# Optimization experiments

Hardware: AMD Instinct MI355X
Metric: run time of the kernel (lower is better)

Reference implementation:

```python
import jax, jax.numpy as jnp
import numpy as np

B, I, H1, H2, E, T = 16384, 512, 256, 128, 8, 2


def setup_inputs() -> dict:
    key = jax.random.key(0)
    ks = jax.random.split(key, 4)
    # Xavier-ish scaling for stability
    x = jax.random.normal(ks[0], (B, I), dtype=jnp.float32)
    W1 = jax.random.normal(ks[1], (E, I, H1), dtype=jnp.float32) / np.sqrt(I)
    b1 = jnp.zeros((E, H1), dtype=jnp.float32)
    W2 = jax.random.normal(ks[2], (E, H1, H2), dtype=jnp.float32) / np.sqrt(H1)
    b2 = jnp.zeros((E, H2), dtype=jnp.float32)
    Wg = jax.random.normal(ks[3], (T, I, E), dtype=jnp.float32) / np.sqrt(I)
    bg = jnp.zeros((T, E), dtype=jnp.float32)
    return {"x": x, "W1": W1, "b1": b1, "W2": W2, "b2": b2, "Wg": Wg, "bg": bg}


def reference(x, W1, b1, W2, b2, Wg, bg):
    # All experts as one grouped GEMM: [E, B, H1]
    h = jax.nn.relu(jnp.einsum('bi,eih->ebh', x, W1) + b1[:, None, :])
    # Last expert layer (lastlayer_reg=True -> act applied): [E, B, H2]
    e_out = jax.nn.relu(jnp.einsum('ebh,eho->ebo', h, W2) + b2[:, None, :])
    # Per-task gates with softmax over experts: [T, B, E]
    gates = jax.nn.softmax(jnp.einsum('bi,tie->tbe', x, Wg) + bg[:, None, :], axis=-1)
    # Gate-weighted combine of expert outputs: [T, B, H2]
    towers = jnp.einsum('tbe,ebo->tbo', gates, e_out)
    return towers
```

## Files before the change

kernel.cpp:

```cpp
#include <hip/hip_runtime.h>
#include <hip/hip_bf16.h>

#define B_  16384
#define I_  512
#define H1_ 256
#define H2_ 128
#define E_  8
#define T_  2

typedef __attribute__((ext_vector_type(8))) short short8;
typedef __attribute__((ext_vector_type(4))) float float4_t;

__device__ inline unsigned short f2bf(float f) {
    union { float f; unsigned u; } v; v.f = f;
    unsigned r = v.u + 0x7FFFu + ((v.u >> 16) & 1u);
    return (unsigned short)(r >> 16);
}

__device__ inline void async_copy16(const unsigned short* g, unsigned short* l) {
    __builtin_amdgcn_global_load_lds(
        (const __attribute__((address_space(1))) void*)g,
        (__attribute__((address_space(3))) void*)l,
        16, 0, 0);
}

__global__ void prep_gates_kernel(const float* __restrict__ x,
                                  unsigned short* __restrict__ xb,
                                  const float* __restrict__ W1,
                                  unsigned short* __restrict__ w1t,
                                  const float* __restrict__ W2,
                                  unsigned short* __restrict__ w2t,
                                  const float* __restrict__ Wg,
                                  const float* __restrict__ bg,
                                  float* __restrict__ gates) {
    __shared__ __align__(16) char smem[16 * 520 * 2 + 4 * 16 * 16 * 4];
    int bid = blockIdx.x;
    int t = threadIdx.x;

    if (bid < 1024) {
        unsigned short* wgtL = (unsigned short*)smem;
        float (*red)[16][16] = (float (*)[16][16])(smem + 16 * 520 * 2);
#pragma unroll
        for (int j = 0; j < 32; ++j) {
            int idx = j * 256 + t;
            int e = idx & 7, i = (idx >> 3) & 511, task = idx >> 12;
            wgtL[(task * 8 + e) * 520 + i] = f2bf(Wg[idx]);
        }
        __syncthreads();

        int w = t >> 6, lane = t & 63;
        int col = lane & 15, quad = lane >> 4;
        int b0 = bid * 16;
        int k0 = w * 128;
        const float* xr = x + (size_t)(b0 + col) * I_ + k0 + quad * 8;
        unsigned short* xw = xb + (size_t)(b0 + col) * I_ + k0 + quad * 8;
        const unsigned short* bL = &wgtL[col * 520 + k0 + quad * 8];
        float4_t acc = {0.f, 0.f, 0.f, 0.f};
#pragma unroll
        for (int ks = 0; ks < 128; ks += 32) {
            float4_t xa = *(const float4_t*)(xr + ks);
            float4_t xc = *(const float4_t*)(xr + ks + 4);
            short8 a;
            a[0] = (short)f2bf(xa[0]); a[1] = (short)f2bf(xa[1]);
            a[2] = (short)f2bf(xa[2]); a[3] = (short)f2bf(xa[3]);
            a[4] = (short)f2bf(xc[0]); a[5] = (short)f2bf(xc[1]);
            a[6] = (short)f2bf(xc[2]); a[7] = (short)f2bf(xc[3]);
            *(short8*)(xw + ks) = a;
            short8 b = *(const short8*)(bL + ks);
            acc = __builtin_amdgcn_mfma_f32_16x16x32_bf16(a, b, acc, 0, 0, 0);
        }
#pragma unroll
        for (int p = 0; p < 4; ++p)
            red[w][quad * 4 + p][col] = acc[p];
        __syncthreads();
        int r = t >> 4, te = t & 15;
        float v = red[0][r][te] + red[1][r][te] + red[2][r][te] + red[3][r][te] + bg[te];
        float m = v;
        m = fmaxf(m, __shfl_xor(m, 1));
        m = fmaxf(m, __shfl_xor(m, 2));
        m = fmaxf(m, __shfl_xor(m, 4));
        float ev = __expf(v - m);
        float s = ev;
        s += __shfl_xor(s, 1);
        s += __shfl_xor(s, 2);
        s += __shfl_xor(s, 4);
        gates[(size_t)te * B_ + b0 + r] = ev / s;
    } else {
        float (*tile)[33] = (float (*)[33])smem;
        const float* in; unsigned short* outp; int R, C, e, r0, c0;
        if (bid < 2048) {
            int tl = bid - 1024;
            e = tl >> 7; int rem = tl & 127;
            R = I_; C = H1_;
            r0 = (rem >> 3) * 32; c0 = (rem & 7) * 32;
            in = W1; outp = w1t;
        } else {
            int tl = bid - 2048;
            e = tl >> 5; int rem = tl & 31;
            R = H1_; C = H2_;
            r0 = (rem >> 2) * 32; c0 = (rem & 3) * 32;
            in = W2; outp = w2t;
        }
        const float* inp = in + (size_t)e * R * C;
        unsigned short* op = outp + (size_t)e * R * C;
        int tx = t & 31, ty = t >> 5;
#pragma unroll
        for (int j = 0; j < 32; j += 8)
            tile[ty + j][tx] = inp[(size_t)(r0 + ty + j) * C + c0 + tx];
        __syncthreads();
#pragma unroll
        for (int j = 0; j < 32; j += 8)
            op[(size_t)(c0 + ty + j) * R + r0 + tx] = f2bf(tile[tx][ty + j]);
    }
}

__global__ __launch_bounds__(512, 2)
void l1_gemm_kernel(const unsigned short* __restrict__ xb,
                    const unsigned short* __restrict__ w1t,
                    const float* __restrict__ b1,
                    unsigned short* __restrict__ h) {
    __shared__ __align__(16) unsigned short smem[65536];

    int bid = blockIdx.x;
    int wg = (bid & 7) * 64 + (bid >> 3);
    int m0 = (wg >> 3) * 256;
    int e  = wg & 7;

    int t = threadIdx.x, w = t >> 6, lane = t & 63;
    int col = lane & 15, quad = lane >> 4;
    int wm = (w & 1) * 128;
    int wn = (w >> 1) * 64;

    int rowA = w * 8 + (lane >> 3);
    int csw  = ((lane & 7) ^ (rowA & 7)) * 8;
    const unsigned short* aG = xb  + (size_t)(m0 + rowA) * I_ + csw;
    const unsigned short* bG = w1t + ((size_t)e * H1_ + rowA) * I_ + csw;

    unsigned short* AsBase = smem;
    unsigned short* BsBase = smem + 32768;
    int ldsw = w * 512;

    float4_t acc[8][4];
#pragma unroll
    for (int mf = 0; mf < 8; ++mf)
#pragma unroll
        for (int nf = 0; nf < 4; ++nf)
            acc[mf][nf] = (float4_t){0.f, 0.f, 0.f, 0.f};

#pragma unroll
    for (int p = 0; p < 4; ++p) {
        async_copy16(aG + ((size_t)p * 64) * I_, AsBase + p * 4096 + ldsw);
        async_copy16(bG + ((size_t)p * 64) * I_, BsBase + p * 4096 + ldsw);
    }

    short8 bf[4][2];

#pragma unroll 1
    for (int kt = 0; kt < 8; ++kt) {
        const int cur = kt & 1, nb = cur ^ 1;
        unsigned short* Ac = AsBase + cur * 16384;
        unsigned short* Bc = BsBase + cur * 16384;
        unsigned short* An = AsBase + nb * 16384;
        unsigned short* Bn = BsBase + nb * 16384;
        const unsigned short* aN = aG + (size_t)(kt + 1) * 64;
        const unsigned short* bN = bG + (size_t)(kt + 1) * 64;

        if (kt < 7) {
            async_copy16(aN, An + ldsw);
            async_copy16(bN, Bn + ldsw);
            asm volatile("s_waitcnt vmcnt(2)" ::: "memory");
        } else {
            asm volatile("s_waitcnt vmcnt(0)" ::: "memory");
        }
        asm volatile("s_barrier" ::: "memory");

#pragma unroll
        for (int nf = 0; nf < 4; ++nf) {
            int n = wn + nf * 16 + col;
#pragma unroll
            for (int kq = 0; kq < 2; ++kq) {
                int q = kq * 4 + quad;
                bf[nf][kq] = *(const short8*)&Bc[n * 64 + ((q ^ (n & 7)) << 3)];
            }
        }

#pragma unroll
        for (int p = 0; p < 4; ++p) {
            if (p > 0 && kt < 7) {
                async_copy16(aN + ((size_t)p * 64) * I_, An + p * 4096 + ldsw);
                async_copy16(bN + ((size_t)p * 64) * I_, Bn + p * 4096 + ldsw);
            }
            short8 af[2][2];
#pragma unroll
            for (int s = 0; s < 2; ++s) {
                int r = wm + (p * 2 + s) * 16 + col;
#pragma unroll
                for (int kq = 0; kq < 2; ++kq) {
                    int q = kq * 4 + quad;
                    af[s][kq] = *(const short8*)&Ac[r * 64 + ((q ^ (r & 7)) << 3)];
                }
            }
            asm volatile("s_waitcnt lgkmcnt(0)" ::: "memory");
            __builtin_amdgcn_sched_barrier(0);
            __builtin_amdgcn_s_setprio(1);
#pragma unroll
            for (int s = 0; s < 2; ++s)
#pragma unroll
                for (int nf = 0; nf < 4; ++nf)
#pragma unroll
                    for (int kq = 0; kq < 2; ++kq)
                        acc[p * 2 + s][nf] = __builtin_amdgcn_mfma_f32_16x16x32_bf16(
                            af[s][kq], bf[nf][kq], acc[p * 2 + s][nf], 0, 0, 0);
            __builtin_amdgcn_s_setprio(0);
            asm volatile("s_barrier" ::: "memory");
        }
    }

    unsigned short* Ct = smem;
    const float* bE = b1 + e * H1_;
#pragma unroll
    for (int half = 0; half < 2; ++half) {
        if ((w & 1) == half) {
#pragma unroll
            for (int mf = 0; mf < 8; ++mf) {
#pragma unroll
                for (int nf = 0; nf < 4; ++nf) {
                    int n = wn + nf * 16 + col;
                    float bv = bE[n];
#pragma unroll
                    for (int p2 = 0; p2 < 4; ++p2) {
                        float v = acc[mf][nf][p2] + bv;
                        v = v > 0.f ? v : 0.f;
                        Ct[(mf * 16 + quad * 4 + p2) * 264 + n] = f2bf(v);
                    }
                }
            }
        }
        __syncthreads();
        unsigned short* hrow = h + ((size_t)e * B_ + m0 + half * 128) * H1_;
#pragma unroll
        for (int j = 0; j < 8; ++j) {
            int idx = j * 512 + t;
            int row = idx >> 5, cc = idx & 31;
            short8 vv = *(const short8*)&Ct[row * 264 + cc * 8];
            *(short8*)&hrow[(size_t)row * H1_ + cc * 8] = vv;
        }
        __syncthreads();
    }
}

__global__ __launch_bounds__(512, 2)
void fused_l2_combine_kernel(const unsigned short* __restrict__ h,
                             const unsigned short* __restrict__ w2t,
                             const float* __restrict__ b2,
                             const float* __restrict__ gates,
                             float* __restrict__ out) {
    __shared__ unsigned short As[64 * 256];
    __shared__ unsigned short Bs[128 * 256];
    __shared__ float gL[16][64];

    int b0 = blockIdx.x * 64;
    int t = threadIdx.x, w = t >> 6, lane = t & 63;
    int col = lane & 15, quad = lane >> 4;
    int wm = (w & 1) * 32, wn = (w >> 1) * 32;

    if (t < 256) {
        int te = t >> 4, r4 = (t & 15) * 4;
        *(float4_t*)&gL[te][r4] = *(const float4_t*)&gates[(size_t)te * B_ + b0 + r4];
    }

    float4_t tw0[2][2], tw1[2][2];
#pragma unroll
    for (int mi = 0; mi < 2; ++mi)
#pragma unroll
        for (int ni = 0; ni < 2; ++ni) {
            tw0[mi][ni] = (float4_t){0.f, 0.f, 0.f, 0.f};
            tw1[mi][ni] = (float4_t){0.f, 0.f, 0.f, 0.f};
        }

    int rL = w * 2 + (lane >> 5);
    int cL = lane & 31;

    for (int e = 0; e < E_; ++e) {
        const unsigned short* hE  = h   + ((size_t)e * B_ + b0) * H1_;
        const unsigned short* w2E = w2t + (size_t)e * H2_ * H1_;

#pragma unroll
        for (int j = 0; j < 4; ++j) {
            int r = j * 16 + rL;
            int cg = (cL & 24) | ((cL ^ r) & 7);
            async_copy16(hE + (size_t)r * H1_ + cg * 8, As + j * 4096 + w * 512);
        }
#pragma unroll
        for (int j = 0; j < 8; ++j) {
            int r = j * 16 + rL;
            int cg = (cL & 24) | ((cL ^ r) & 7);
            async_copy16(w2E + (size_t)r * H1_ + cg * 8, Bs + j * 4096 + w * 512);
        }
        __syncthreads();

        float4_t acc[2][2];
#pragma unroll
        for (int mi = 0; mi < 2; ++mi)
#pragma unroll
            for (int ni = 0; ni < 2; ++ni)
                acc[mi][ni] = (float4_t){0.f, 0.f, 0.f, 0.f};

#pragma unroll
        for (int kk = 0; kk < 8; ++kk) {
            int c = kk * 4 + quad;
            short8 af[2], bfv[2];
#pragma unroll
            for (int mi = 0; mi < 2; ++mi) {
                int r = wm + mi * 16 + col;
                int l = (c & 24) | ((c ^ r) & 7);
                af[mi] = *(const short8*)&As[r * 256 + l * 8];
            }
#pragma unroll
            for (int ni = 0; ni < 2; ++ni) {
                int n = wn + ni * 16 + col;
                int l = (c & 24) | ((c ^ n) & 7);
                bfv[ni] = *(const short8*)&Bs[n * 256 + l * 8];
            }
#pragma unroll
            for (int mi = 0; mi < 2; ++mi)
#pragma unroll
                for (int ni = 0; ni < 2; ++ni)
                    acc[mi][ni] = __builtin_amdgcn_mfma_f32_16x16x32_bf16(
                        af[mi], bfv[ni], acc[mi][ni], 0, 0, 0);
        }
        __syncthreads();

#pragma unroll
        for (int ni = 0; ni < 2; ++ni) {
            float bv = b2[e * H2_ + wn + ni * 16 + col];
#pragma unroll
            for (int mi = 0; mi < 2; ++mi) {
#pragma unroll
                for (int p = 0; p < 4; ++p) {
                    int rloc = wm + mi * 16 + quad * 4 + p;
                    float v = acc[mi][ni][p] + bv;
                    v = v > 0.f ? v : 0.f;
                    tw0[mi][ni][p] += gL[e][rloc] * v;
                    tw1[mi][ni][p] += gL[8 + e][rloc] * v;
                }
            }
        }
    }

#pragma unroll
    for (int mi = 0; mi < 2; ++mi) {
#pragma unroll
        for (int ni = 0; ni < 2; ++ni) {
            int n = wn + ni * 16 + col;
#pragma unroll
            for (int p = 0; p < 4; ++p) {
                int r = b0 + wm + mi * 16 + quad * 4 + p;
                out[(size_t)r * H2_ + n] = tw0[mi][ni][p];
                out[(size_t)B_ * H2_ + (size_t)r * H2_ + n] = tw1[mi][ni][p];
            }
        }
    }
}

extern "C" void kernel_launch(void* const* d_in, const int* in_sizes, int n_in,
                              void* d_out, int out_size, void* d_ws, size_t ws_size,
                              hipStream_t stream) {
    const float* x  = (const float*)d_in[0];
    const float* W1 = (const float*)d_in[1];
    const float* b1 = (const float*)d_in[2];
    const float* W2 = (const float*)d_in[3];
    const float* b2 = (const float*)d_in[4];
    const float* Wg = (const float*)d_in[5];
    const float* bg = (const float*)d_in[6];
    float* out = (float*)d_out;

    char* ws = (char*)d_ws;
    unsigned short* xb    = (unsigned short*)(ws);
    unsigned short* w1t   = (unsigned short*)(ws + 16777216);
    unsigned short* w2t   = (unsigned short*)(ws + 18874368);
    float*          gates = (float*)(ws + 19398656);
    unsigned short* h     = (unsigned short*)(ws + 20447232);

    prep_gates_kernel<<<dim3(2304), 256, 0, stream>>>(x, xb, W1, w1t, W2, w2t, Wg, bg, gates);

    l1_gemm_kernel<<<dim3(512), 512, 0, stream>>>(xb, w1t, b1, h);

    fused_l2_combine_kernel<<<dim3(B_ / 64), 512, 0, stream>>>(h, w2t, b2, gates, out);
}
```

Before: 168.2 us.

## Pipeline L2 combine kernel with 3-slot async K-chunk ring and simplify L1 loop

The fused L2/combine kernel now streams each expert's H1 dimension in 64-wide chunks through a three-slot LDS ring with async global-to-LDS copies, so the next chunk's loads overlap the current chunk's MFMAs instead of a load-all-then-compute step per expert. This shrinks LDS use and raises the launch-bounds occupancy hint from 2 to 4 blocks. The L1 GEMM issues all next-tile prefetches up front and reads all A/B fragments per k-quarter with one barrier per k-tile, dropping the per-subtile interleaving and barriers. The trade-offs are more register pressure in L1 and more barriers per expert in L2.

```diff
diff --git a/kernel.cpp b/kernel.cpp
--- a/kernel.cpp
+++ b/kernel.cpp
@@ -131,13 +131,13 @@
     int wm = (w & 1) * 128;
     int wn = (w >> 1) * 64;
 
-    int rowA = w * 8 + (lane >> 3);
-    int csw  = ((lane & 7) ^ (rowA & 7)) * 8;
+    int rowA = t >> 3;
+    int csw  = ((t & 7) ^ (rowA & 7)) * 8;
     const unsigned short* aG = xb  + (size_t)(m0 + rowA) * I_ + csw;
     const unsigned short* bG = w1t + ((size_t)e * H1_ + rowA) * I_ + csw;
 
-    unsigned short* AsBase = smem;
-    unsigned short* BsBase = smem + 32768;
+    unsigned short* As = smem;
+    unsigned short* Bs = smem + 32768;
     int ldsw = w * 512;
 
     float4_t acc[8][4];
@@ -149,71 +149,56 @@
 
 #pragma unroll
     for (int p = 0; p < 4; ++p) {
-        async_copy16(aG + ((size_t)p * 64) * I_, AsBase + p * 4096 + ldsw);
-        async_copy16(bG + ((size_t)p * 64) * I_, BsBase + p * 4096 + ldsw);
-    }
-
-    short8 bf[4][2];
+        async_copy16(aG + ((size_t)p * 64) * I_, As + p * 4096 + ldsw);
+        async_copy16(bG + ((size_t)p * 64) * I_, Bs + p * 4096 + ldsw);
+    }
 
 #pragma unroll 1
     for (int kt = 0; kt < 8; ++kt) {
-        const int cur = kt & 1, nb = cur ^ 1;
-        unsigned short* Ac = AsBase + cur * 16384;
-        unsigned short* Bc = BsBase + cur * 16384;
-        unsigned short* An = AsBase + nb * 16384;
-        unsigned short* Bn = BsBase + nb * 16384;
-        const unsigned short* aN = aG + (size_t)(kt + 1) * 64;
-        const unsigned short* bN = bG + (size_t)(kt + 1) * 64;
+        const int cur = kt & 1;
+        const unsigned short* Ac = As + cur * 16384;
+        const unsigned short* Bc = Bs + cur * 16384;
 
         if (kt < 7) {
-            async_copy16(aN, An + ldsw);
-            async_copy16(bN, Bn + ldsw);
-            asm volatile("s_waitcnt vmcnt(2)" ::: "memory");
+            unsigned short* An = As + (cur ^ 1) * 16384;
+            unsigned short* Bn = Bs + (cur ^ 1) * 16384;
+            const unsigned short* aN = aG + (size_t)(kt + 1) * 64;
+            const unsigned short* bN = bG + (size_t)(kt + 1) * 64;
+#pragma unroll
+            for (int p = 0; p < 4; ++p) {
+                async_copy16(aN + ((size_t)p * 64) * I_, An + p * 4096 + ldsw);
+                async_copy16(bN + ((size_t)p * 64) * I_, Bn + p * 4096 + ldsw);
+            }
+            asm volatile("s_waitcnt vmcnt(8)" ::: "memory");
         } else {
             asm volatile("s_waitcnt vmcnt(0)" ::: "memory");
         }
         asm volatile("s_barrier" ::: "memory");
 
 #pragma unroll
-        for (int nf = 0; nf < 4; ++nf) {
-            int n = wn + nf * 16 + col;
-#pragma unroll
-            for (int kq = 0; kq < 2; ++kq) {
-                int q = kq * 4 + quad;
-                bf[nf][kq] = *(const short8*)&Bc[n * 64 + ((q ^ (n & 7)) << 3)];
-            }
-        }
-
-#pragma unroll
-        for (int p = 0; p < 4; ++p) {
-            if (p > 0 && kt < 7) {
-                async_copy16(aN + ((size_t)p * 64) * I_, An + p * 4096 + ldsw);
-                async_copy16(bN + ((size_t)p * 64) * I_, Bn + p * 4096 + ldsw);
-            }
-            short8 af[2][2];
-#pragma unroll
-            for (int s = 0; s < 2; ++s) {
-                int r = wm + (p * 2 + s) * 16 + col;
-#pragma unroll
-                for (int kq = 0; kq < 2; ++kq) {
-                    int q = kq * 4 + quad;
-                    af[s][kq] = *(const short8*)&Ac[r * 64 + ((q ^ (r & 7)) << 3)];
-                }
-            }
-            asm volatile("s_waitcnt lgkmcnt(0)" ::: "memory");
-            __builtin_amdgcn_sched_barrier(0);
+        for (int kq = 0; kq < 2; ++kq) {
+            int q = kq * 4 + quad;
+            short8 af[8], bfv[4];
+#pragma unroll
+            for (int mf = 0; mf < 8; ++mf) {
+                int r = wm + mf * 16 + col;
+                af[mf] = *(const short8*)&Ac[r * 64 + ((q ^ (r & 7)) << 3)];
+            }
+#pragma unroll
+            for (int nf = 0; nf < 4; ++nf) {
+                int n = wn + nf * 16 + col;
+                bfv[nf] = *(const short8*)&Bc[n * 64 + ((q ^ (n & 7)) << 3)];
+            }
             __builtin_amdgcn_s_setprio(1);
 #pragma unroll
-            for (int s = 0; s < 2; ++s)
+            for (int mf = 0; mf < 8; ++mf)
 #pragma unroll
                 for (int nf = 0; nf < 4; ++nf)
-#pragma unroll
-                    for (int kq = 0; kq < 2; ++kq)
-                        acc[p * 2 + s][nf] = __builtin_amdgcn_mfma_f32_16x16x32_bf16(
-                            af[s][kq], bf[nf][kq], acc[p * 2 + s][nf], 0, 0, 0);
+                    acc[mf][nf] = __builtin_amdgcn_mfma_f32_16x16x32_bf16(
+                        af[mf], bfv[nf], acc[mf][nf], 0, 0, 0);
             __builtin_amdgcn_s_setprio(0);
-            asm volatile("s_barrier" ::: "memory");
-        }
+        }
+        asm volatile("s_barrier" ::: "memory");
     }
 
     unsigned short* Ct = smem;
@@ -249,15 +234,17 @@
     }
 }
 
-__global__ __launch_bounds__(512, 2)
+__global__ __launch_bounds__(512, 4)
 void fused_l2_combine_kernel(const unsigned short* __restrict__ h,
                              const unsigned short* __restrict__ w2t,
                              const float* __restrict__ b2,
                              const float* __restrict__ gates,
                              float* __restrict__ out) {
-    __shared__ unsigned short As[64 * 256];
-    __shared__ unsigned short Bs[128 * 256];
+    __shared__ __align__(16) unsigned short ring[36864];
     __shared__ float gL[16][64];
+
+    unsigned short* Aslot = ring;
+    unsigned short* Bslot = ring + 12288;
 
     int b0 = blockIdx.x * 64;
     int t = threadIdx.x, w = t >> 6, lane = t & 63;
@@ -269,6 +256,10 @@
         *(float4_t*)&gL[te][r4] = *(const float4_t*)&gates[(size_t)te * B_ + b0 + r4];
     }
 
+    int rowA = t >> 3;
+    int csw  = ((t & 7) ^ (rowA & 7)) * 8;
+    int ldsw = w * 512;
+
     float4_t tw0[2][2], tw1[2][2];
 #pragma unroll
     for (int mi = 0; mi < 2; ++mi)
@@ -278,74 +269,82 @@
             tw1[mi][ni] = (float4_t){0.f, 0.f, 0.f, 0.f};
         }
 
-    int rL = w * 2 + (lane >> 5);
-    int cL = lane & 31;
-
-    for (int e = 0; e < E_; ++e) {
-        const unsigned short* hE  = h   + ((size_t)e * B_ + b0) * H1_;
-        const unsigned short* w2E = w2t + (size_t)e * H2_ * H1_;
-
-#pragma unroll
-        for (int j = 0; j < 4; ++j) {
-            int r = j * 16 + rL;
-            int cg = (cL & 24) | ((cL ^ r) & 7);
-            async_copy16(hE + (size_t)r * H1_ + cg * 8, As + j * 4096 + w * 512);
-        }
-#pragma unroll
-        for (int j = 0; j < 8; ++j) {
-            int r = j * 16 + rL;
-            int cg = (cL & 24) | ((cL ^ r) & 7);
-            async_copy16(w2E + (size_t)r * H1_ + cg * 8, Bs + j * 4096 + w * 512);
-        }
-        __syncthreads();
-
-        float4_t acc[2][2];
-#pragma unroll
-        for (int mi = 0; mi < 2; ++mi)
-#pragma unroll
-            for (int ni = 0; ni < 2; ++ni)
-                acc[mi][ni] = (float4_t){0.f, 0.f, 0.f, 0.f};
-
-#pragma unroll
-        for (int kk = 0; kk < 8; ++kk) {
-            int c = kk * 4 + quad;
+    auto stage = [&](int cid, int slot) {
+        int ee = cid >> 2, kc = cid & 3;
+        const unsigned short* hE = h + ((size_t)ee * B_ + b0 + rowA) * H1_ + kc * 64 + csw;
+        async_copy16(hE, Aslot + slot * 4096 + ldsw);
+        const unsigned short* wE = w2t + ((size_t)ee * H2_ + rowA) * H1_ + kc * 64 + csw;
+        async_copy16(wE, Bslot + slot * 8192 + ldsw);
+        async_copy16(wE + (size_t)64 * H1_, Bslot + slot * 8192 + 4096 + ldsw);
+    };
+
+    stage(0, 0);
+
+    float4_t acc[2][2];
+    int rd = 0, wr = 1;
+#pragma unroll 1
+    for (int cid = 0; cid < 32; ++cid) {
+        if (cid < 31) {
+            stage(cid + 1, wr);
+            asm volatile("s_waitcnt vmcnt(3)" ::: "memory");
+        } else {
+            asm volatile("s_waitcnt vmcnt(0)" ::: "memory");
+        }
+        asm volatile("s_barrier" ::: "memory");
+
+        if ((cid & 3) == 0) {
+#pragma unroll
+            for (int mi = 0; mi < 2; ++mi)
+#pragma unroll
+                for (int ni = 0; ni < 2; ++ni)
+                    acc[mi][ni] = (float4_t){0.f, 0.f, 0.f, 0.f};
+        }
+        const unsigned short* Ac = Aslot + rd * 4096;
+        const unsigned short* Bc = Bslot + rd * 8192;
+#pragma unroll
+        for (int kq = 0; kq < 2; ++kq) {
+            int q = kq * 4 + quad;
             short8 af[2], bfv[2];
 #pragma unroll
             for (int mi = 0; mi < 2; ++mi) {
                 int r = wm + mi * 16 + col;
-                int l = (c & 24) | ((c ^ r) & 7);
-                af[mi] = *(const short8*)&As[r * 256 + l * 8];
+                af[mi] = *(const short8*)&Ac[r * 64 + ((q ^ (r & 7)) << 3)];
             }
 #pragma unroll
             for (int ni = 0; ni < 2; ++ni) {
                 int n = wn + ni * 16 + col;
-                int l = (c & 24) | ((c ^ n) & 7);
-                bfv[ni] = *(const short8*)&Bs[n * 256 + l * 8];
-            }
+                bfv[ni] = *(const short8*)&Bc[n * 64 + ((q ^ (n & 7)) << 3)];
+            }
+            __builtin_amdgcn_s_setprio(1);
 #pragma unroll
             for (int mi = 0; mi < 2; ++mi)
 #pragma unroll
                 for (int ni = 0; ni < 2; ++ni)
                     acc[mi][ni] = __builtin_amdgcn_mfma_f32_16x16x32_bf16(
                         af[mi], bfv[ni], acc[mi][ni], 0, 0, 0);
-        }
-        __syncthreads();
-
-#pragma unroll
-        for (int ni = 0; ni < 2; ++ni) {
-            float bv = b2[e * H2_ + wn + ni * 16 + col];
-#pragma unroll
-            for (int mi = 0; mi < 2; ++mi) {
-#pragma unroll
-                for (int p = 0; p < 4; ++p) {
-                    int rloc = wm + mi * 16 + quad * 4 + p;
-                    float v = acc[mi][ni][p] + bv;
-                    v = v > 0.f ? v : 0.f;
-                    tw0[mi][ni][p] += gL[e][rloc] * v;
-                    tw1[mi][ni][p] += gL[8 + e][rloc] * v;
+            __builtin_amdgcn_s_setprio(0);
+        }
+
+        if ((cid & 3) == 3) {
+            int ee = cid >> 2;
+#pragma unroll
+            for (int ni = 0; ni < 2; ++ni) {
+                float bv = b2[ee * H2_ + wn + ni * 16 + col];
+#pragma unroll
+                for (int mi = 0; mi < 2; ++mi) {
+#pragma unroll
+                    for (int p = 0; p < 4; ++p) {
+                        int rloc = wm + mi * 16 + quad * 4 + p;
+                        float v = acc[mi][ni][p] + bv;
+                        v = v > 0.f ? v : 0.f;
+                        tw0[mi][ni][p] += gL[ee][rloc] * v;
+                        tw1[mi][ni][p] += gL[8 + ee][rloc] * v;
+                    }
                 }
             }
         }
+        rd = (rd == 2) ? 0 : rd + 1;
+        wr = (wr == 2) ? 0 : wr + 1;
     }
 
 #pragma unroll
```

Measured after the change: 163.6 us. 2.8% less time.
